# Performance work log

Measured on AMD Instinct MI355X. Metric: run time of the kernel, lower is better.

The kernel has to match this reference:

```python
import jax, jax.numpy as jnp
import numpy as np

WS = 10                      # window radius
K = 2 * WS + 1               # 21
K2 = K * K                   # 441 window positions
SIG_COLOR = 1.0 / (0.1 * 0.1 * 2.0)
SIG_SPACE = 1.0 / (7.0 * 7.0 * 2.0)
LP = 0.8
C1 = 10.0
C2 = 5.0
ALPHA = 5.0
EPS = 1e-6


def _patches(img):
    """torch nn.Unfold(kernel_size=image_size, padding=WS) trick: returns the
    K2 zero-padded shifted copies of the image, shape (b, K2, c, h, w)."""
    b, c, h, w = img.shape
    p = jax.lax.conv_general_dilated_patches(img, (K, K), (1, 1), [(WS, WS), (WS, WS)])
    # (b, c*K2, h, w) with channel-major (c, ky, kx) ordering -> (b, K2, c, h, w)
    return p.reshape(b, c, K2, h, w).transpose(0, 2, 1, 3, 4)


def _edge_response(img):
    # local contrast: sum over window and channels of |I_j - I_i| (zero-padded
    # / non-positive neighbors masked out), shape (b, h, w)
    p = _patches(img)
    d = jnp.where(p > 0, p - img[:, None], 0.0)
    return jnp.abs(d).sum(axis=(1, 2))


def setup_inputs() -> dict:
    key = jax.random.key(0)
    k1, k2 = jax.random.split(key)
    original_images = jax.random.uniform(k1, (1, 3, 224, 224), dtype=jnp.float32)
    smooth_images = jax.random.uniform(k2, (1, 3, 224, 224), dtype=jnp.float32)
    return {"original_images": original_images, "smooth_images": smooth_images}


def reference(original_images, smooth_images):
    b, c, h, w = smooth_images.shape

    # ti_minus_tj: |T_j - T_i| with zero/non-positive padded neighbors zeroed;
    # the shifted copies are detached in the original (stop_gradient)
    sp = jax.lax.stop_gradient(_patches(smooth_images))
    ti = jnp.abs(jnp.where(sp > 0, sp - smooth_images[:, None], 0.0))  # (b,K2,c,h,w)

    # edge-response based region masks
    er_o = _edge_response(original_images)
    er_s = _edge_response(smooth_images)
    use_large = ((er_o < C1) & (er_s - er_o > C2))[:, None, None]  # (b,1,1,h,w)

    # spatial affinity ws (constant gaussian over window offsets)
    dy = jnp.arange(-WS, WS + 1)
    ws = jnp.exp(-SIG_SPACE * (dy[:, None] ** 2 + dy[None, :] ** 2).astype(jnp.float32))
    ws = ws.reshape(1, K2, 1, 1, 1)

    # color affinity wr from the guidance (original) image; note the original
    # code computes the affinity BEFORE masking the color difference, so the
    # affinity includes zero-padded neighbors -- replicated faithfully
    op = jax.lax.stop_gradient(_patches(original_images))
    cd = ((op - original_images[:, None]) ** 2).sum(axis=2, keepdims=True)  # (b,K2,1,h,w)
    wr = jnp.exp(-SIG_COLOR * cd)

    ws = jnp.where(use_large, ws, 0.0)
    wr = jnp.where(~use_large, wr, 0.0)

    scale = 1.0 / (h * w * b) / (WS * WS)  # note: window_size**2, not K2 (quirk kept)
    return scale * jnp.sum(ALPHA * ws * ti ** 2 + wr * (ti + EPS) ** LP)
```

## Files before the change

### kernel.cpp

```cpp
#include <hip/hip_runtime.h>


#define WSR 10
#define KK  21
#define HH  224
#define WW  224
#define HWSZ (HH*WW)
#define SIG_COLOR 50.0f
#define LPW 0.8f
#define C1T 10.0f
#define C2T 5.0f
#define ALPHA_W 5.0f
#define EPSV 1e-6f
#define LOG2E 1.44269504088896f
#define NSC (-SIG_COLOR * LOG2E)
#define SSP ((1.0f/98.0f) * LOG2E)

#define TX 32
#define TY 2
#define HALO_W (TX + 2*WSR)
#define HALO_H (TY + 2*WSR)
#define HSZ (HALO_W * HALO_H)
#define NBX (WW / TX)
#define NBY (HH / TY)
#define NBLK (NBX * NBY)
#define NTHR 448
#define SCALEF (1.0f / ((float)HWSZ * 100.0f))
#define EPS_CORR (1323.0f * EPSV)

__device__ __forceinline__ float fexp2(float x) { return __builtin_amdgcn_exp2f(x); }
__device__ __forceinline__ float flog2(float x) { return __builtin_amdgcn_logf(x); }

template<bool B> struct BoolC { static constexpr bool value = B; };

static constexpr float WXT[KK] = {
  0.3604486f, 0.4375650f, 0.5204496f, 0.6065307f, 0.6925675f,
  0.7748383f, 0.8493658f, 0.9122539f, 0.9600054f, 0.9898479f,
  1.0f,
  0.9898479f, 0.9600054f, 0.9122539f, 0.8493658f, 0.7748383f,
  0.6925675f, 0.6065307f, 0.5204496f, 0.4375650f, 0.3604486f };

__global__ __launch_bounds__(NTHR) void smooth_loss_fused(
    const float* __restrict__ orig, const float* __restrict__ smo,
    float* __restrict__ out)
{
    __shared__ float2 tA[HSZ];
    __shared__ float2 tB[HSZ];
    __shared__ float2 tC[HSZ];
    __shared__ float racc0[NTHR], racc1[NTHR], racc2[NTHR], racc3[NTHR];

    const int tid = threadIdx.x;
    const int bid = blockIdx.x;
    const int bx  = bid % NBX;
    const int by  = bid / NBX;

    const int gx0 = bx * TX - WSR;
    const int gy0 = by * TY - WSR;
    for (int i = tid; i < HSZ; i += NTHR) {
        int r = i / HALO_W;
        int c = i - r * HALO_W;
        int gy = gy0 + r, gx = gx0 + c;
        bool v = ((unsigned)gy < (unsigned)HH) & ((unsigned)gx < (unsigned)WW);
        int gi = gy * WW + gx;
        float o0=0.f,o1=0.f,o2=0.f,s0=0.f,s1=0.f,s2=0.f;
        if (v) {
            o0 = orig[gi]; o1 = orig[gi+HWSZ]; o2 = orig[gi+2*HWSZ];
            s0 = smo[gi];  s1 = smo[gi+HWSZ]; s2 = smo[gi+2*HWSZ];
        }
        tA[i] = make_float2(o0,o1);
        tB[i] = make_float2(o2,s0);
        tC[i] = make_float2(s1,s2);
    }
    __syncthreads();

    const int lane = tid & 63;
    const int wv   = tid >> 6;
    const int pr   = lane >> 5;
    const int pc   = lane & 31;

    const int cpos = (WSR + pr) * HALO_W + (WSR + pc);
    const float2 cA = tA[cpos], cB = tB[cpos], cC = tC[cpos];
    const float oc0=cA.x, oc1=cA.y, oc2=cB.x, sc0=cB.y, sc1=cC.x, sc2=cC.y;

    float er_o=0.f, er_u=0.f, sl=0.f, ss=0.f;

    const bool interior = (bx >= 1) & (bx <= 5) & (by >= 5) & (by <= 106);

    auto scan = [&](auto mc) {
        constexpr bool MASKED = decltype(mc)::value;
        #pragma unroll 1
        for (int r = 0; r < 3; ++r) {
            const int ky = wv + 7 * r;
            const float dyf = (float)(ky - WSR);
            const float wy = fexp2(-SSP * dyf * dyf);
            const int rbase = (pr + ky) * HALO_W + pc;
            const float2* __restrict__ rA = &tA[rbase];
            const float2* __restrict__ rB = &tB[rbase];
            const float2* __restrict__ rC = &tC[rbase];
            float srow = 0.f;
            #pragma unroll
            for (int kx = 0; kx < KK; ++kx) {
                float2 A = rA[kx];
                float2 B = rB[kx];
                float2 C = rC[kx];
                float e0 = A.x - oc0, e1 = A.y - oc1, e2 = B.x - oc2;
                float d0 = B.y - sc0, d1 = C.x - sc1, d2 = C.y - sc2;
                if constexpr (MASKED) {
                    e0 = (A.x > 0.f) ? e0 : 0.f;
                    e1 = (A.y > 0.f) ? e1 : 0.f;
                    e2 = (B.x > 0.f) ? e2 : 0.f;
                    d0 = (B.y > 0.f) ? d0 : 0.f;
                    d1 = (C.x > 0.f) ? d1 : 0.f;
                    d2 = (C.y > 0.f) ? d2 : 0.f;
                }
                er_o += fabsf(e0); er_o += fabsf(e1); er_o += fabsf(e2);
                float cd = fmaf(e2, e2, fmaf(e1, e1, e0*e0));
                float g  = NSC * cd;
                float u0 = fabsf(d0) + EPSV;
                float u1 = fabsf(d1) + EPSV;
                float u2 = fabsf(d2) + EPSV;
                er_u += u0; er_u += u1; er_u += u2;
                float tt = fmaf(d2, d2, fmaf(d1, d1, d0*d0));
                srow = fmaf(WXT[kx], tt, srow);
                float q0 = fexp2(fmaf(LPW, flog2(u0), g));
                float q1 = fexp2(fmaf(LPW, flog2(u1), g));
                float q2 = fexp2(fmaf(LPW, flog2(u2), g));
                ss += q0; ss += q1; ss += q2;
            }
            sl = fmaf(wy, srow, sl);
        }
    };
    if (interior) scan(BoolC<false>{});
    else          scan(BoolC<true>{});

    racc0[tid]=er_o; racc1[tid]=er_u; racc2[tid]=sl; racc3[tid]=ss;
    __syncthreads();

    if (tid < 64) {
        float eo=0.f, es=0.f, l=0.f, s=0.f;
        #pragma unroll
        for (int k = 0; k < 7; ++k) {
            int idx = tid + 64 * k;
            eo += racc0[idx]; es += racc1[idx];
            l  += racc2[idx]; s  += racc3[idx];
        }
        es -= EPS_CORR;
        bool use_large = (eo < C1T) && ((es - eo) > C2T);
        float contrib = use_large ? (ALPHA_W * l) : s;
        #pragma unroll
        for (int off = 32; off > 0; off >>= 1)
            contrib += __shfl_down(contrib, off, 64);
        if (tid == 0)
            atomicAdd(out, contrib * SCALEF);
    }
}

extern "C" void kernel_launch(void* const* d_in, const int* in_sizes, int n_in,
                              void* d_out, int out_size, void* d_ws, size_t ws_size,
                              hipStream_t stream) {
    const float* orig = (const float*)d_in[0];
    const float* smo  = (const float*)d_in[1];
    float* out = (float*)d_out;

    hipMemsetAsync(d_out, 0, sizeof(float), stream);
    smooth_loss_fused<<<NBLK, NTHR, 0, stream>>>(orig, smo, out);
}
```

Baseline: 95.71 us.

## Split horizontal window between two half-waves and halve tile width

Halves the tile width to 16 pixels and gives the two 32-lane halves of each wavefront separate halves of the 21-wide horizontal window (11 taps each, the 11th masked out for the upper half). The grid doubles in block count while per-thread serial work per row drops from 21 to 11 taps, raising parallelism and occupancy across the CUs. In exchange it adds a padding element in shared memory, one wasted tap per row for half the lanes, more halo reloads per output pixel, and a modified reduction over 14 partials per pixel.

```diff
diff --git a/kernel.cpp b/kernel.cpp
--- a/kernel.cpp
+++ b/kernel.cpp
@@ -16,7 +16,7 @@
 #define NSC (-SIG_COLOR * LOG2E)
 #define SSP ((1.0f/98.0f) * LOG2E)
 
-#define TX 32
+#define TX 16
 #define TY 2
 #define HALO_W (TX + 2*WSR)
 #define HALO_H (TY + 2*WSR)
@@ -44,9 +44,9 @@
     const float* __restrict__ orig, const float* __restrict__ smo,
     float* __restrict__ out)
 {
-    __shared__ float2 tA[HSZ];
-    __shared__ float2 tB[HSZ];
-    __shared__ float2 tC[HSZ];
+    __shared__ float2 tA[HSZ + 1];
+    __shared__ float2 tB[HSZ + 1];
+    __shared__ float2 tC[HSZ + 1];
     __shared__ float racc0[NTHR], racc1[NTHR], racc2[NTHR], racc3[NTHR];
 
     const int tid = threadIdx.x;
@@ -71,12 +71,26 @@
         tB[i] = make_float2(o2,s0);
         tC[i] = make_float2(s1,s2);
     }
+    if (tid == 0) {
+        tA[HSZ] = make_float2(0.f,0.f);
+        tB[HSZ] = make_float2(0.f,0.f);
+        tC[HSZ] = make_float2(0.f,0.f);
+    }
     __syncthreads();
 
     const int lane = tid & 63;
     const int wv   = tid >> 6;
-    const int pr   = lane >> 5;
-    const int pc   = lane & 31;
+    const int pc   = lane & 15;
+    const int pr   = (lane >> 4) & 1;
+    const int kh   = lane >> 5;
+    const int kxb  = kh * 11;
+    const float kmsk = (kh == 0) ? 1.f : 0.f;
+
+    float wxl[11];
+    #pragma unroll
+    for (int i = 0; i < 10; ++i)
+        wxl[i] = kh ? WXT[11 + i] : WXT[i];
+    wxl[10] = kh ? 0.f : WXT[10];
 
     const int cpos = (WSR + pr) * HALO_W + (WSR + pc);
     const float2 cA = tA[cpos], cB = tB[cpos], cC = tC[cpos];
@@ -84,7 +98,7 @@
 
     float er_o=0.f, er_u=0.f, sl=0.f, ss=0.f;
 
-    const bool interior = (bx >= 1) & (bx <= 5) & (by >= 5) & (by <= 106);
+    const bool interior = (bx >= 1) & (bx <= 12) & (by >= 5) & (by <= 106);
 
     auto scan = [&](auto mc) {
         constexpr bool MASKED = decltype(mc)::value;
@@ -93,16 +107,16 @@
             const int ky = wv + 7 * r;
             const float dyf = (float)(ky - WSR);
             const float wy = fexp2(-SSP * dyf * dyf);
-            const int rbase = (pr + ky) * HALO_W + pc;
+            const int rbase = (pr + ky) * HALO_W + pc + kxb;
             const float2* __restrict__ rA = &tA[rbase];
             const float2* __restrict__ rB = &tB[rbase];
             const float2* __restrict__ rC = &tC[rbase];
             float srow = 0.f;
             #pragma unroll
-            for (int kx = 0; kx < KK; ++kx) {
-                float2 A = rA[kx];
-                float2 B = rB[kx];
-                float2 C = rC[kx];
+            for (int kxi = 0; kxi < 11; ++kxi) {
+                float2 A = rA[kxi];
+                float2 B = rB[kxi];
+                float2 C = rC[kxi];
                 float e0 = A.x - oc0, e1 = A.y - oc1, e2 = B.x - oc2;
                 float d0 = B.y - sc0, d1 = C.x - sc1, d2 = C.y - sc2;
                 if constexpr (MASKED) {
@@ -113,19 +127,26 @@
                     d1 = (C.x > 0.f) ? d1 : 0.f;
                     d2 = (C.y > 0.f) ? d2 : 0.f;
                 }
-                er_o += fabsf(e0); er_o += fabsf(e1); er_o += fabsf(e2);
+                float ae = (fabsf(e0) + fabsf(e1)) + fabsf(e2);
                 float cd = fmaf(e2, e2, fmaf(e1, e1, e0*e0));
                 float g  = NSC * cd;
                 float u0 = fabsf(d0) + EPSV;
                 float u1 = fabsf(d1) + EPSV;
                 float u2 = fabsf(d2) + EPSV;
-                er_u += u0; er_u += u1; er_u += u2;
+                float us = (u0 + u1) + u2;
                 float tt = fmaf(d2, d2, fmaf(d1, d1, d0*d0));
-                srow = fmaf(WXT[kx], tt, srow);
+                srow = fmaf(wxl[kxi], tt, srow);
                 float q0 = fexp2(fmaf(LPW, flog2(u0), g));
                 float q1 = fexp2(fmaf(LPW, flog2(u1), g));
                 float q2 = fexp2(fmaf(LPW, flog2(u2), g));
-                ss += q0; ss += q1; ss += q2;
+                float qs = (q0 + q1) + q2;
+                if (kxi == 10) {
+                    er_o = fmaf(kmsk, ae, er_o);
+                    er_u = fmaf(kmsk, us, er_u);
+                    ss   = fmaf(kmsk, qs, ss);
+                } else {
+                    er_o += ae; er_u += us; ss += qs;
+                }
             }
             sl = fmaf(wy, srow, sl);
         }
@@ -136,11 +157,11 @@
     racc0[tid]=er_o; racc1[tid]=er_u; racc2[tid]=sl; racc3[tid]=ss;
     __syncthreads();
 
-    if (tid < 64) {
+    if (tid < 32) {
         float eo=0.f, es=0.f, l=0.f, s=0.f;
         #pragma unroll
-        for (int k = 0; k < 7; ++k) {
-            int idx = tid + 64 * k;
+        for (int m = 0; m < 14; ++m) {
+            int idx = tid + 32 * m;
             eo += racc0[idx]; es += racc1[idx];
             l  += racc2[idx]; s  += racc3[idx];
         }
@@ -148,7 +169,7 @@
         bool use_large = (eo < C1T) && ((es - eo) > C2T);
         float contrib = use_large ? (ALPHA_W * l) : s;
         #pragma unroll
-        for (int off = 32; off > 0; off >>= 1)
+        for (int off = 16; off > 0; off >>= 1)
             contrib += __shfl_down(contrib, off, 64);
         if (tid == 0)
             atomicAdd(out, contrib * SCALEF);
```

Result: slower. 105.3 us (+10.0%).
